# Kernel optimization log

Hardware: AMD Instinct MI355X
Metric: run time of the kernel (lower is better)

The kernel has to match this reference:

```python
import jax, jax.numpy as jnp
import numpy as np

N, E, DIN, DH, DOUT = 50000, 800000, 128, 256, 128
EPS = 1e-5
SLOPE = 0.01  # torch leaky_relu default


def setup_inputs() -> dict:
    key = jax.random.key(0)
    ks = jax.random.split(key, 8)
    w = lambda k, shape: jax.random.normal(k, shape, jnp.float32) * 0.05
    return {
        "x": jax.random.normal(ks[0], (N, DIN), jnp.float32),
        "edge_index": jax.random.randint(ks[1], (2, E), 0, N, jnp.int32),
        "W0": w(ks[2], (DH, DIN)),  "b0": jnp.zeros((DH,), jnp.float32),
        "g0": jnp.ones((DH,), jnp.float32), "be0": jnp.zeros((DH,), jnp.float32),
        "W1": w(ks[3], (DH, DH)),   "b1": jnp.zeros((DH,), jnp.float32),
        "g1": jnp.ones((DH,), jnp.float32), "be1": jnp.zeros((DH,), jnp.float32),
        "W2": w(ks[4], (DOUT, DH)), "b2": jnp.zeros((DOUT,), jnp.float32),
        "g2": jnp.ones((DOUT,), jnp.float32), "be2": jnp.zeros((DOUT,), jnp.float32),
    }


def _gcn_forward(x, edge_index, params):
    n = x.shape[0]
    loop = jnp.arange(n, dtype=edge_index.dtype)
    src = jnp.concatenate([edge_index[0], loop])  # add self-loops
    dst = jnp.concatenate([edge_index[1], loop])
    deg = jnp.zeros((n,), x.dtype).at[dst].add(1.0)
    dinv = jax.lax.rsqrt(deg)  # deg >= 1 due to self-loops
    enorm = (dinv[src] * dinv[dst])[:, None]  # [E+N, 1]

    def conv(h, W, b):
        h = h @ W.T  # linear first (PyG GCNConv), messages in out_dim
        msg = h[src] * enorm
        return jax.ops.segment_sum(msg, dst, num_segments=n) + b

    def bn(h, g, be):  # BatchNorm1d, training-mode batch stats (biased var)
        mu = h.mean(0)
        var = ((h - mu) ** 2).mean(0)
        return (h - mu) * jax.lax.rsqrt(var + EPS) * g + be

    (W0, b0, g0, be0, W1, b1, g1, be1, W2, b2, g2, be2) = params
    h = jax.nn.leaky_relu(bn(conv(x, W0, b0), g0, be0), SLOPE)
    h = jax.nn.leaky_relu(bn(conv(h, W1, b1), g1, be1), SLOPE)
    h = bn(conv(h, W2, b2), g2, be2)  # last layer: no leaky_relu
    return h


def reference(x, edge_index, W0, b0, g0, be0, W1, b1, g1, be1, W2, b2, g2, be2):
    return _gcn_forward(x, edge_index,
                        (W0, b0, g0, be0, W1, b1, g1, be1, W2, b2, g2, be2))
```

## Files before the change

### kernel.cpp

```cpp
#include <hip/hip_runtime.h>
#include <hip/hip_bf16.h>

#define N_NODES 50000
#define N_EDGES 800000
#define DIN 128
#define DH   256
#define DOUT 128
#define EPSV 1e-5f
#define SLOPE 0.01f
#define SCAN_NB ((N_NODES + 255) / 256)

typedef __bf16 bf16x8 __attribute__((ext_vector_type(8)));
typedef __bf16 bf16x4 __attribute__((ext_vector_type(4)));
typedef float  f32x4  __attribute__((ext_vector_type(4)));

__global__ void cast_kernel(const float* __restrict__ src, __bf16* __restrict__ dst, int n4) {
    int i = blockIdx.x * blockDim.x + threadIdx.x;
    if (i < n4) {
        float4 v = ((const float4*)src)[i];
        bf16x4 o; o[0] = (__bf16)v.x; o[1] = (__bf16)v.y; o[2] = (__bf16)v.z; o[3] = (__bf16)v.w;
        ((bf16x4*)dst)[i] = o;
    }
}

__global__ void cast_scale_kernel(const float* __restrict__ src, const float* __restrict__ dinv,
                                  __bf16* __restrict__ dst) {
    int i = blockIdx.x * blockDim.x + threadIdx.x;
    if (i < N_NODES * DIN / 8) {
        int row = i / (DIN / 8);
        float d = dinv[row];
        float4 a = ((const float4*)src)[i * 2];
        float4 b = ((const float4*)src)[i * 2 + 1];
        bf16x8 o;
        o[0] = (__bf16)(a.x * d); o[1] = (__bf16)(a.y * d);
        o[2] = (__bf16)(a.z * d); o[3] = (__bf16)(a.w * d);
        o[4] = (__bf16)(b.x * d); o[5] = (__bf16)(b.y * d);
        o[6] = (__bf16)(b.z * d); o[7] = (__bf16)(b.w * d);
        ((bf16x8*)dst)[i] = o;
    }
}

__global__ void deg_kernel(const int* __restrict__ dst, int* __restrict__ deg) {
    int i = blockIdx.x * blockDim.x + threadIdx.x;
    if (i < N_EDGES) atomicAdd(&deg[dst[i]], 1);
}

__global__ void dinv_kernel(const int* __restrict__ deg, float* __restrict__ dinv) {
    int i = blockIdx.x * blockDim.x + threadIdx.x;
    if (i < N_NODES) dinv[i] = rsqrtf((float)deg[i] + 1.0f);
}

__global__ __launch_bounds__(256) void scan_bsum(const int* __restrict__ deg,
                                                 int* __restrict__ bsum) {
    __shared__ int lds[256];
    int i = blockIdx.x * 256 + threadIdx.x;
    lds[threadIdx.x] = (i < N_NODES) ? deg[i] + 1 : 0;
    __syncthreads();
    #pragma unroll
    for (int off = 128; off > 0; off >>= 1) {
        if (threadIdx.x < off) lds[threadIdx.x] += lds[threadIdx.x + off];
        __syncthreads();
    }
    if (threadIdx.x == 0) bsum[blockIdx.x] = lds[0];
}

__global__ __launch_bounds__(256) void scan_boffs(const int* __restrict__ bsum,
                                                  int* __restrict__ boffs) {
    __shared__ int lds[256];
    const int t = threadIdx.x;
    lds[t] = (t < SCAN_NB) ? bsum[t] : 0;
    __syncthreads();
    #pragma unroll
    for (int off = 1; off < 256; off <<= 1) {
        int add = (t >= off) ? lds[t - off] : 0;
        __syncthreads();
        lds[t] += add;
        __syncthreads();
    }
    boffs[t] = (t == 0) ? 0 : lds[t - 1];
}

__global__ __launch_bounds__(256) void scan_write(const int* __restrict__ deg,
                                                  const int* __restrict__ boffs,
                                                  int* __restrict__ rp) {
    __shared__ int lds[256];
    const int t = threadIdx.x;
    int i = blockIdx.x * 256 + t;
    int v = (i < N_NODES) ? deg[i] + 1 : 0;
    lds[t] = v;
    __syncthreads();
    #pragma unroll
    for (int off = 1; off < 256; off <<= 1) {
        int add = (t >= off) ? lds[t - off] : 0;
        __syncthreads();
        lds[t] += add;
        __syncthreads();
    }
    if (i < N_NODES) rp[i] = boffs[blockIdx.x] + lds[t] - v;
    if (i == N_NODES - 1) rp[N_NODES] = boffs[blockIdx.x] + lds[t];
}

__global__ void scatter_kernel(const int* __restrict__ ei,
                               const int* __restrict__ rp, int* __restrict__ cursor,
                               int* __restrict__ csr) {
    int e = blockIdx.x * blockDim.x + threadIdx.x;
    if (e >= N_EDGES + N_NODES) return;
    int pos, src;
    if (e < N_EDGES) {
        src = ei[e]; int dst = ei[N_EDGES + e];
        pos = rp[dst] + atomicAdd(&cursor[dst], 1);
    } else {
        src = e - N_EDGES;
        pos = rp[src + 1] - 1;
    }
    csr[pos] = src;
}

template<int C8, int SLICES, bool OUTF32>
__global__ __launch_bounds__(256) void spmm_sl(const int* __restrict__ rp,
                                               const int* __restrict__ csr,
                                               const float* __restrict__ dinv,
                                               const __bf16* __restrict__ h,
                                               void* __restrict__ outp) {
    constexpr int C = C8 * 8;
    constexpr int LPS = C8 / SLICES;
    constexpr int RPB = 256 / LPS;
    const int slice = blockIdx.x % SLICES;
    const int chunk = blockIdx.x / SLICES;
    const int r = chunk * RPB + threadIdx.x / LPS;
    const int l = slice * LPS + threadIdx.x % LPS;
    if (r >= N_NODES) return;
    const bf16x8* __restrict__ h8 = (const bf16x8*)h;
    const int e0 = rp[r], e1 = rp[r + 1];
    float acc0[8] = {}, acc1[8] = {};
    int e = e0;
    for (; e + 8 <= e1; e += 8) {
        int p[8];
        #pragma unroll
        for (int u = 0; u < 8; ++u) p[u] = csr[e + u];
        bf16x8 v[8];
        #pragma unroll
        for (int u = 0; u < 8; ++u) v[u] = h8[(long)p[u] * C8 + l];
        #pragma unroll
        for (int u = 0; u < 8; ++u) {
            #pragma unroll
            for (int j = 0; j < 8; ++j) {
                if (u & 1) acc1[j] += (float)v[u][j];
                else       acc0[j] += (float)v[u][j];
            }
        }
    }
    for (; e + 2 <= e1; e += 2) {
        int p0 = csr[e], p1 = csr[e + 1];
        bf16x8 v0 = h8[(long)p0 * C8 + l];
        bf16x8 v1 = h8[(long)p1 * C8 + l];
        #pragma unroll
        for (int j = 0; j < 8; ++j) {
            acc0[j] += (float)v0[j];
            acc1[j] += (float)v1[j];
        }
    }
    if (e < e1) {
        int p0 = csr[e];
        bf16x8 v0 = h8[(long)p0 * C8 + l];
        #pragma unroll
        for (int j = 0; j < 8; ++j) acc0[j] += (float)v0[j];
    }
    const float d = dinv[r];
    float res[8];
    #pragma unroll
    for (int j = 0; j < 8; ++j) res[j] = (acc0[j] + acc1[j]) * d;
    if (OUTF32) {
        float* o = (float*)outp + (long)r * C + l * 8;
        ((float4*)o)[0] = make_float4(res[0], res[1], res[2], res[3]);
        ((float4*)o)[1] = make_float4(res[4], res[5], res[6], res[7]);
    } else {
        bf16x8 ob;
        #pragma unroll
        for (int j = 0; j < 8; ++j) ob[j] = (__bf16)res[j];
        ((bf16x8*)outp)[(long)r * C8 + l] = ob;
    }
}

template<int K, int NC, bool FUSE_BN, bool RELU, bool SCALE>
__global__ __launch_bounds__(256) void gemm_tile(const __bf16* __restrict__ A,
                                                 const __bf16* __restrict__ W,
                                                 const float* __restrict__ ss,
                                                 const float* __restrict__ dinv,
                                                 __bf16* __restrict__ C,
                                                 int M) {
    constexpr int NW = NC / 64;
    constexpr int MW = 4 / NW;
    constexpr int BM = MW * 64;
    constexpr int NSTEP = K / 32;
    __shared__ __bf16 As[2][BM][40];

    const int tid = threadIdx.x;
    const int wave = tid >> 6, lane = tid & 63;
    const int ln15 = lane & 15, kg = lane >> 4;
    const int wm = wave / NW, wn = wave % NW;
    const int m0 = blockIdx.x * BM;
    const int srow = tid >> 2, schunk = tid & 3;

    int grow[MW];
    #pragma unroll
    for (int p = 0; p < MW; ++p) {
        int gr = m0 + p * 64 + srow;
        grow[p] = gr < M ? gr : M - 1;
    }

    f32x4 acc[4][4];
    #pragma unroll
    for (int i = 0; i < 4; ++i)
        #pragma unroll
        for (int j = 0; j < 4; ++j) acc[i][j] = (f32x4){0.f, 0.f, 0.f, 0.f};

#define LOAD_A(vv, kt_)                                                         \
    _Pragma("unroll")                                                           \
    for (int p = 0; p < MW; ++p)                                                \
        vv[p] = *(const bf16x8*)(A + (long)grow[p] * K + (kt_) + schunk * 8);

#define XFORM_A(vv, kt_)                                                        \
    if (FUSE_BN) {                                                              \
        const f32x4* ss4 = (const f32x4*)ss;                                    \
        int ci = ((kt_) + schunk * 8) >> 2;                                     \
        f32x4 sc0 = ss4[ci],            sc1 = ss4[ci + 1];                      \
        f32x4 sh0 = ss4[(K >> 2) + ci], sh1 = ss4[(K >> 2) + ci + 1];           \
        _Pragma("unroll")                                                       \
        for (int p = 0; p < MW; ++p) {                                          \
            float f[8];                                                         \
            _Pragma("unroll")                                                   \
            for (int j = 0; j < 4; ++j) {                                       \
                f[j]     = fmaf((float)vv[p][j],     sc0[j], sh0[j]);           \
                f[j + 4] = fmaf((float)vv[p][j + 4], sc1[j], sh1[j]);           \
            }                                                                   \
            if (RELU) {                                                         \
                _Pragma("unroll")                                               \
                for (int j = 0; j < 8; ++j) f[j] = f[j] > 0.f ? f[j] : SLOPE * f[j]; \
            }                                                                   \
            _Pragma("unroll")                                                   \
            for (int j = 0; j < 8; ++j) vv[p][j] = (__bf16)f[j];                \
        }                                                                       \
    }

#define WRITE_A(buf, vv)                                                        \
    _Pragma("unroll")                                                           \
    for (int p = 0; p < MW; ++p)                                                \
        *(bf16x8*)(&As[buf][p * 64 + srow][schunk * 8]) = vv[p];

    bf16x8 v0[MW], v[MW];
    LOAD_A(v0, 0)
    XFORM_A(v0, 0)
    WRITE_A(0, v0)
    if (NSTEP > 1) {
        LOAD_A(v, 32)
        XFORM_A(v, 32)
    }
    __syncthreads();

    int cur = 0;
    #pragma unroll
    for (int step = 0; step < NSTEP; ++step) {
        const int kt = step * 32;
        if (step + 1 < NSTEP) {
            WRITE_A(cur ^ 1, v)
        }
        bf16x8 vn[MW];
        if (step + 2 < NSTEP) {
            LOAD_A(vn, kt + 64)
        }
        bf16x8 b[4];
        #pragma unroll
        for (int j = 0; j < 4; ++j)
            b[j] = *(const bf16x8*)(W + (long)(wn * 64 + j * 16 + ln15) * K + kt + kg * 8);
        #pragma unroll
        for (int i = 0; i < 4; ++i) {
            bf16x8 a = *(const bf16x8*)(&As[cur][wm * 64 + i * 16 + ln15][kg * 8]);
            #pragma unroll
            for (int j = 0; j < 4; ++j)
                acc[i][j] = __builtin_amdgcn_mfma_f32_16x16x32_bf16(a, b[j], acc[i][j], 0, 0, 0);
        }
        if (step + 2 < NSTEP) {
            XFORM_A(vn, kt + 64)
            #pragma unroll
            for (int p = 0; p < MW; ++p) v[p] = vn[p];
        }
        __syncthreads();
        cur ^= 1;
    }
#undef LOAD_A
#undef XFORM_A
#undef WRITE_A

    #pragma unroll
    for (int i = 0; i < 4; ++i) {
        #pragma unroll
        for (int q = 0; q < 4; ++q) {
            int r = m0 + wm * 64 + i * 16 + kg * 4 + q;
            if (r < M) {
                float d = SCALE ? dinv[r] : 1.0f;
                #pragma unroll
                for (int j = 0; j < 4; ++j)
                    C[(long)r * NC + wn * 64 + j * 16 + ln15] = (__bf16)(acc[i][j][q] * d);
            }
        }
    }
}

#define NB_STATS 128
template<int C, bool BF16>
__global__ __launch_bounds__(256) void bn_stats(const void* __restrict__ hp,
                                                float* __restrict__ partial) {
    constexpr int LPR = C / 4;
    constexpr int RPI = 256 / LPR;
    const int chunk = threadIdx.x % LPR;
    const int rof   = threadIdx.x / LPR;
    float s[4] = {}, s2[4] = {};
    for (int r = blockIdx.x * RPI + rof; r < N_NODES; r += NB_STATS * RPI) {
        float v[4];
        if (BF16) {
            bf16x4 x = ((const bf16x4*)hp)[(long)r * LPR + chunk];
            #pragma unroll
            for (int j = 0; j < 4; ++j) v[j] = (float)x[j];
        } else {
            float4 x = ((const float4*)hp)[(long)r * LPR + chunk];
            v[0] = x.x; v[1] = x.y; v[2] = x.z; v[3] = x.w;
        }
        #pragma unroll
        for (int j = 0; j < 4; ++j) { s[j] += v[j]; s2[j] += v[j] * v[j]; }
    }
    __shared__ float red[256 * 8];
    #pragma unroll
    for (int j = 0; j < 4; ++j) { red[threadIdx.x * 8 + j] = s[j]; red[threadIdx.x * 8 + 4 + j] = s2[j]; }
    __syncthreads();
    if (rof == 0) {
        #pragma unroll
        for (int g = 1; g < RPI; ++g) {
            #pragma unroll
            for (int j = 0; j < 4; ++j) {
                s[j]  += red[(g * LPR + chunk) * 8 + j];
                s2[j] += red[(g * LPR + chunk) * 8 + 4 + j];
            }
        }
        #pragma unroll
        for (int j = 0; j < 4; ++j) {
            partial[blockIdx.x * 2 * C + chunk * 4 + j]     = s[j];
            partial[blockIdx.x * 2 * C + C + chunk * 4 + j] = s2[j];
        }
    }
}

template<int C>
__global__ void bn_reduce(const float* __restrict__ partial, const float* __restrict__ g,
                          const float* __restrict__ be, float* __restrict__ ss) {
    int c = threadIdx.x;
    float s_0 = 0.f, s_1 = 0.f, q_0 = 0.f, q_1 = 0.f;
    #pragma unroll 4
    for (int b = 0; b < NB_STATS; b += 2) {
        s_0 += partial[b * 2 * C + c];
        q_0 += partial[b * 2 * C + C + c];
        s_1 += partial[(b + 1) * 2 * C + c];
        q_1 += partial[(b + 1) * 2 * C + C + c];
    }
    float s = s_0 + s_1, s2 = q_0 + q_1;
    const float invn = 1.0f / (float)N_NODES;
    float mean = s * invn;
    float var  = s2 * invn - mean * mean;
    float rstd = rsqrtf(var + EPSV);
    float sc = g[c] * rstd;
    ss[c] = sc;
    ss[C + c] = be[c] - mean * sc;
}

template<int C>
__global__ __launch_bounds__(256) void bn_apply_f32(float* __restrict__ h,
                                                    const float* __restrict__ ss) {
    constexpr int LPR = C / 4;
    const long total = (long)N_NODES * LPR;
    const long stride = (long)gridDim.x * blockDim.x;
    for (long idx = (long)blockIdx.x * blockDim.x + threadIdx.x; idx < total; idx += stride) {
        int chunk = (int)(idx % LPR);
        float4 sc = ((const float4*)ss)[chunk];
        float4 sh = ((const float4*)(ss + C))[chunk];
        float4 x = ((float4*)h)[idx];
        x.x = fmaf(x.x, sc.x, sh.x); x.y = fmaf(x.y, sc.y, sh.y);
        x.z = fmaf(x.z, sc.z, sh.z); x.w = fmaf(x.w, sc.w, sh.w);
        ((float4*)h)[idx] = x;
    }
}

extern "C" void kernel_launch(void* const* d_in, const int* in_sizes, int n_in,
                              void* d_out, int out_size, void* d_ws, size_t ws_size,
                              hipStream_t stream) {
    const float* x   = (const float*)d_in[0];
    const int*   ei  = (const int*)  d_in[1];
    const float* W0  = (const float*)d_in[2];
    const float* g0  = (const float*)d_in[4];
    const float* be0 = (const float*)d_in[5];
    const float* W1  = (const float*)d_in[6];
    const float* g1  = (const float*)d_in[8];
    const float* be1 = (const float*)d_in[9];
    const float* W2  = (const float*)d_in[10];
    const float* g2  = (const float*)d_in[12];
    const float* be2 = (const float*)d_in[13];
    float* out = (float*)d_out;

    char* wsb = (char*)d_ws;
    auto alloc = [&](size_t bytes) { char* p = wsb; wsb += (bytes + 255) & ~255UL; return p; };
    int*    deg     = (int*)   alloc(N_NODES * 4);
    int*    rp      = (int*)   alloc((N_NODES + 4) * 4);
    int*    cursor  = (int*)   alloc(N_NODES * 4);
    float*  dinv    = (float*) alloc(N_NODES * 4);
    int*    bsum    = (int*)   alloc(256 * 4);
    int*    boffs   = (int*)   alloc(257 * 4);
    float*  partial = (float*) alloc(NB_STATS * 2 * DH * 4);
    float*  ss      = (float*) alloc(2 * DH * 4);
    int*    csr     = (int*)   alloc((size_t)(N_EDGES + N_NODES) * 4);
    __bf16* w0b     = (__bf16*)alloc(DH * DIN * 2);
    __bf16* w1b     = (__bf16*)alloc(DH * DH * 2);
    __bf16* w2b     = (__bf16*)alloc(DOUT * DH * 2);
    __bf16* xb      = (__bf16*)alloc((size_t)N_NODES * DIN * 2);
    __bf16* bf0     = (__bf16*)alloc((size_t)N_NODES * DH * 2);
    __bf16* bf1     = (__bf16*)alloc((size_t)N_NODES * DH * 2);

    cast_kernel<<<(DH * DIN / 4 + 255) / 256, 256, 0, stream>>>(W0, w0b, DH * DIN / 4);
    cast_kernel<<<(DH * DH  / 4 + 255) / 256, 256, 0, stream>>>(W1, w1b, DH * DH / 4);
    cast_kernel<<<(DOUT * DH / 4 + 255) / 256, 256, 0, stream>>>(W2, w2b, DOUT * DH / 4);

    hipMemsetAsync(deg, 0, N_NODES * 4, stream);
    hipMemsetAsync(cursor, 0, N_NODES * 4, stream);
    deg_kernel<<<(N_EDGES + 255) / 256, 256, 0, stream>>>(ei + N_EDGES, deg);
    dinv_kernel<<<(N_NODES + 255) / 256, 256, 0, stream>>>(deg, dinv);
    scan_bsum<<<SCAN_NB, 256, 0, stream>>>(deg, bsum);
    scan_boffs<<<1, 256, 0, stream>>>(bsum, boffs);
    scan_write<<<SCAN_NB, 256, 0, stream>>>(deg, boffs, rp);
    scatter_kernel<<<(N_EDGES + N_NODES + 255) / 256, 256, 0, stream>>>(ei, rp, cursor, csr);

    cast_scale_kernel<<<(N_NODES * (DIN / 8) + 255) / 256, 256, 0, stream>>>(x, dinv, xb);

    constexpr int RPB = 64;
    const int nchunks = (N_NODES + RPB - 1) / RPB;

    spmm_sl<DIN / 8, 4, false><<<nchunks * 4, 256, 0, stream>>>(rp, csr, dinv, xb, bf0);
    gemm_tile<DIN, DH, false, false, false><<<(N_NODES + 63) / 64, 256, 0, stream>>>(
        bf0, w0b, nullptr, nullptr, bf1, N_NODES);
    bn_stats<DH, true><<<NB_STATS, 256, 0, stream>>>(bf1, partial);
    bn_reduce<DH><<<1, DH, 0, stream>>>(partial, g0, be0, ss);

    gemm_tile<DH, DH, true, true, true><<<(N_NODES + 63) / 64, 256, 0, stream>>>(
        bf1, w1b, ss, dinv, bf0, N_NODES);
    spmm_sl<DH / 8, 8, false><<<nchunks * 8, 256, 0, stream>>>(rp, csr, dinv, bf0, bf1);
    bn_stats<DH, true><<<NB_STATS, 256, 0, stream>>>(bf1, partial);
    bn_reduce<DH><<<1, DH, 0, stream>>>(partial, g1, be1, ss);

    gemm_tile<DH, DOUT, true, true, true><<<(N_NODES + 127) / 128, 256, 0, stream>>>(
        bf1, w2b, ss, dinv, bf0, N_NODES);
    spmm_sl<DOUT / 8, 4, true><<<nchunks * 4, 256, 0, stream>>>(rp, csr, dinv, bf0, out);
    bn_stats<DOUT, false><<<NB_STATS, 256, 0, stream>>>(out, partial);
    bn_reduce<DOUT><<<1, DOUT, 0, stream>>>(partial, g2, be2, ss);
    bn_apply_f32<DOUT><<<2048, 256, 0, stream>>>(out, ss);
}
```

Before: 439.0 us.

## Store SpMM gather inputs in column-sliced layout for compact per-slice working sets

The producers of the SpMM inputs (the cast/scale kernel and the GEMMs before SpMM) now write their output in a slice-major layout: each 32-column slice of all nodes is stored contiguously. Each SpMM slice block therefore gathers from a compact region rather than strided 64-byte pieces of wide rows, which is meant to improve L2/MALL locality for the random neighbour gathers. CSR index loads are also made nontemporal to keep them from evicting feature data. The GEMM epilogue writes become more scattered, and the layout ties SLICES to the template parameters, which must stay consistent.

```diff
diff --git a/kernel.cpp b/kernel.cpp
--- a/kernel.cpp
+++ b/kernel.cpp
@@ -23,14 +23,19 @@
     }
 }
 
-__global__ void cast_scale_kernel(const float* __restrict__ src, const float* __restrict__ dinv,
-                                  __bf16* __restrict__ dst) {
+__global__ void cast_scale_slice_kernel(const float* __restrict__ src,
+                                        const float* __restrict__ dinv,
+                                        __bf16* __restrict__ dst) {
     int i = blockIdx.x * blockDim.x + threadIdx.x;
-    if (i < N_NODES * DIN / 8) {
-        int row = i / (DIN / 8);
-        float d = dinv[row];
-        float4 a = ((const float4*)src)[i * 2];
-        float4 b = ((const float4*)src)[i * 2 + 1];
+    if (i < N_NODES * (DIN / 8)) {
+        int ch = i & 3;
+        int sr = i >> 2;
+        int r  = sr % N_NODES;
+        int s  = sr / N_NODES;
+        float d = dinv[r];
+        int base_f4 = r * (DIN / 4) + s * 8 + ch * 2;
+        float4 a = ((const float4*)src)[base_f4];
+        float4 b = ((const float4*)src)[base_f4 + 1];
         bf16x8 o;
         o[0] = (__bf16)(a.x * d); o[1] = (__bf16)(a.y * d);
         o[2] = (__bf16)(a.z * d); o[3] = (__bf16)(a.w * d);
@@ -128,19 +133,19 @@
     const int slice = blockIdx.x % SLICES;
     const int chunk = blockIdx.x / SLICES;
     const int r = chunk * RPB + threadIdx.x / LPS;
-    const int l = slice * LPS + threadIdx.x % LPS;
+    const int lw = threadIdx.x % LPS;
     if (r >= N_NODES) return;
-    const bf16x8* __restrict__ h8 = (const bf16x8*)h;
+    const bf16x8* __restrict__ h8 = (const bf16x8*)h + (long)slice * N_NODES * LPS + lw;
     const int e0 = rp[r], e1 = rp[r + 1];
     float acc0[8] = {}, acc1[8] = {};
     int e = e0;
     for (; e + 8 <= e1; e += 8) {
         int p[8];
         #pragma unroll
-        for (int u = 0; u < 8; ++u) p[u] = csr[e + u];
+        for (int u = 0; u < 8; ++u) p[u] = __builtin_nontemporal_load(csr + e + u);
         bf16x8 v[8];
         #pragma unroll
-        for (int u = 0; u < 8; ++u) v[u] = h8[(long)p[u] * C8 + l];
+        for (int u = 0; u < 8; ++u) v[u] = h8[(long)p[u] * LPS];
         #pragma unroll
         for (int u = 0; u < 8; ++u) {
             #pragma unroll
@@ -151,9 +156,10 @@
         }
     }
     for (; e + 2 <= e1; e += 2) {
-        int p0 = csr[e], p1 = csr[e + 1];
-        bf16x8 v0 = h8[(long)p0 * C8 + l];
-        bf16x8 v1 = h8[(long)p1 * C8 + l];
+        int p0 = __builtin_nontemporal_load(csr + e);
+        int p1 = __builtin_nontemporal_load(csr + e + 1);
+        bf16x8 v0 = h8[(long)p0 * LPS];
+        bf16x8 v1 = h8[(long)p1 * LPS];
         #pragma unroll
         for (int j = 0; j < 8; ++j) {
             acc0[j] += (float)v0[j];
@@ -161,8 +167,8 @@
         }
     }
     if (e < e1) {
-        int p0 = csr[e];
-        bf16x8 v0 = h8[(long)p0 * C8 + l];
+        int p0 = __builtin_nontemporal_load(csr + e);
+        bf16x8 v0 = h8[(long)p0 * LPS];
         #pragma unroll
         for (int j = 0; j < 8; ++j) acc0[j] += (float)v0[j];
     }
@@ -171,18 +177,18 @@
     #pragma unroll
     for (int j = 0; j < 8; ++j) res[j] = (acc0[j] + acc1[j]) * d;
     if (OUTF32) {
-        float* o = (float*)outp + (long)r * C + l * 8;
+        float* o = (float*)outp + (long)r * C + (slice * LPS + lw) * 8;
         ((float4*)o)[0] = make_float4(res[0], res[1], res[2], res[3]);
         ((float4*)o)[1] = make_float4(res[4], res[5], res[6], res[7]);
     } else {
         bf16x8 ob;
         #pragma unroll
         for (int j = 0; j < 8; ++j) ob[j] = (__bf16)res[j];
-        ((bf16x8*)outp)[(long)r * C8 + l] = ob;
-    }
-}
-
-template<int K, int NC, bool FUSE_BN, bool RELU, bool SCALE>
+        ((bf16x8*)outp)[(long)r * C8 + slice * LPS + lw] = ob;
+    }
+}
+
+template<int K, int NC, bool FUSE_BN, bool RELU, bool SCALE, int SOUT>
 __global__ __launch_bounds__(256) void gemm_tile(const __bf16* __restrict__ A,
                                                  const __bf16* __restrict__ W,
                                                  const float* __restrict__ ss,
@@ -300,8 +306,17 @@
             if (r < M) {
                 float d = SCALE ? dinv[r] : 1.0f;
                 #pragma unroll
-                for (int j = 0; j < 4; ++j)
-                    C[(long)r * NC + wn * 64 + j * 16 + ln15] = (__bf16)(acc[i][j][q] * d);
+                for (int j = 0; j < 4; ++j) {
+                    int col = wn * 64 + j * 16 + ln15;
+                    long addr;
+                    if (SOUT > 0) {
+                        int s = col >> 5, cw = col & 31;
+                        addr = ((long)s * M + r) * 32 + cw;
+                    } else {
+                        addr = (long)r * NC + col;
+                    }
+                    C[addr] = (__bf16)(acc[i][j][q] * d);
+                }
             }
         }
     }
@@ -436,24 +451,23 @@
     scan_write<<<SCAN_NB, 256, 0, stream>>>(deg, boffs, rp);
     scatter_kernel<<<(N_EDGES + N_NODES + 255) / 256, 256, 0, stream>>>(ei, rp, cursor, csr);
 
-    cast_scale_kernel<<<(N_NODES * (DIN / 8) + 255) / 256, 256, 0, stream>>>(x, dinv, xb);
-
-    constexpr int RPB = 64;
-    const int nchunks = (N_NODES + RPB - 1) / RPB;
+    cast_scale_slice_kernel<<<(N_NODES * (DIN / 8) + 255) / 256, 256, 0, stream>>>(x, dinv, xb);
+
+    const int nchunks = (N_NODES + 63) / 64;
 
     spmm_sl<DIN / 8, 4, false><<<nchunks * 4, 256, 0, stream>>>(rp, csr, dinv, xb, bf0);
-    gemm_tile<DIN, DH, false, false, false><<<(N_NODES + 63) / 64, 256, 0, stream>>>(
+    gemm_tile<DIN, DH, false, false, false, 0><<<(N_NODES + 63) / 64, 256, 0, stream>>>(
         bf0, w0b, nullptr, nullptr, bf1, N_NODES);
     bn_stats<DH, true><<<NB_STATS, 256, 0, stream>>>(bf1, partial);
     bn_reduce<DH><<<1, DH, 0, stream>>>(partial, g0, be0, ss);
 
-    gemm_tile<DH, DH, true, true, true><<<(N_NODES + 63) / 64, 256, 0, stream>>>(
+    gemm_tile<DH, DH, true, true, true, 8><<<(N_NODES + 63) / 64, 256, 0, stream>>>(
         bf1, w1b, ss, dinv, bf0, N_NODES);
     spmm_sl<DH / 8, 8, false><<<nchunks * 8, 256, 0, stream>>>(rp, csr, dinv, bf0, bf1);
     bn_stats<DH, true><<<NB_STATS, 256, 0, stream>>>(bf1, partial);
     bn_reduce<DH><<<1, DH, 0, stream>>>(partial, g1, be1, ss);
 
-    gemm_tile<DH, DOUT, true, true, true><<<(N_NODES + 127) / 128, 256, 0, stream>>>(
+    gemm_tile<DH, DOUT, true, true, true, 4><<<(N_NODES + 127) / 128, 256, 0, stream>>>(
         bf1, w2b, ss, dinv, bf0, N_NODES);
     spmm_sl<DOUT / 8, 4, true><<<nchunks * 4, 256, 0, stream>>>(rp, csr, dinv, bf0, out);
     bn_stats<DOUT, false><<<NB_STATS, 256, 0, stream>>>(out, partial);
```

Result: no change. 442.3 us (+0.8%).
